# Optimization experiments

Measured on AMD Instinct MI355X. Metric: run time of the kernel, lower is better.

The kernel has to match this reference:

```python
import jax, jax.numpy as jnp
import numpy as np

SEQ = 4096
D_MODEL = 2048


def setup_inputs() -> dict:
    key = jax.random.key(0)
    k1, k2, k3, k4 = jax.random.split(key, 4)
    scale = 1.0 / np.sqrt(D_MODEL)
    token_encodings = jax.random.normal(k1, (SEQ, D_MODEL), dtype=jnp.float32)
    W_q = jax.random.normal(k2, (D_MODEL, D_MODEL), dtype=jnp.float32) * scale
    W_k = jax.random.normal(k3, (D_MODEL, D_MODEL), dtype=jnp.float32) * scale
    W_v = jax.random.normal(k4, (D_MODEL, D_MODEL), dtype=jnp.float32) * scale
    # causal mask: True where attention is disallowed (strictly upper triangular),
    # mirroring `mask = mask == 0` applied to a lower-triangular ones matrix.
    mask = jnp.triu(jnp.ones((SEQ, SEQ), dtype=bool), k=1)
    return {"token_encodings": token_encodings, "W_q": W_q, "W_k": W_k,
            "W_v": W_v, "mask": mask}


def reference(token_encodings, W_q, W_k, W_v, mask):
    # nn.Linear(bias=False): y = x @ W.T
    q = token_encodings @ W_q.T  # [S, D]
    k = token_encodings @ W_k.T  # [S, D]
    v = token_encodings @ W_v.T  # [S, D]
    sims = q @ k.T               # [S, S]
    scaled = sims / jnp.asarray(np.sqrt(D_MODEL), dtype=sims.dtype)
    scaled = jnp.where(mask, jnp.asarray(-1e9, dtype=scaled.dtype), scaled)
    attn = jax.nn.softmax(scaled, axis=1)
    return attn @ v              # [S, D]
```

## Files before the change

### kernel.cpp

```cpp
#include <hip/hip_runtime.h>
#include <hip/hip_bf16.h>

typedef unsigned short u16;
typedef __attribute__((ext_vector_type(8))) short short8;
typedef __attribute__((ext_vector_type(4))) float f32x4;
typedef __attribute__((ext_vector_type(4))) unsigned short u16x4;

#define SEQL 4096
#define DMOD 2048

__device__ __forceinline__ u16 f2bf(float x) {
    unsigned int u = __float_as_uint(x);
    u += 0x7FFF + ((u >> 16) & 1);
    return (u16)(u >> 16);
}

__device__ __forceinline__ float bf2f(u16 x) {
    return __uint_as_float(((unsigned)x) << 16);
}

__device__ __forceinline__ void async_copy16(const void* g, void* s) {
    __builtin_amdgcn_global_load_lds(
        (const __attribute__((address_space(1))) unsigned int*)g,
        (__attribute__((address_space(3))) unsigned int*)s,
        16, 0, 0);
}

__global__ __launch_bounds__(256)
void cast_f32_bf16(const float* __restrict__ in, u16* __restrict__ out, int n4) {
    int i = blockIdx.x * 256 + threadIdx.x;
    if (i >= n4) return;
    float4 v = ((const float4*)in)[i];
    u16x4 r;
    r[0] = f2bf(v.x); r[1] = f2bf(v.y); r[2] = f2bf(v.z); r[3] = f2bf(v.w);
    ((u16x4*)out)[i] = r;
}

__global__ __launch_bounds__(256)
void cast3_f32_bf16(const float* __restrict__ w0, const float* __restrict__ w1,
                    const float* __restrict__ w2, u16* __restrict__ o0,
                    u16* __restrict__ o1, u16* __restrict__ o2, int n4) {
    int i = blockIdx.x * 256 + threadIdx.x;
    if (i >= n4) return;
    const float* in = blockIdx.y == 0 ? w0 : blockIdx.y == 1 ? w1 : w2;
    u16* out        = blockIdx.y == 0 ? o0 : blockIdx.y == 1 ? o1 : o2;
    float4 v = ((const float4*)in)[i];
    u16x4 r;
    r[0] = f2bf(v.x); r[1] = f2bf(v.y); r[2] = f2bf(v.z); r[3] = f2bf(v.w);
    ((u16x4*)out)[i] = r;
}

__global__ __launch_bounds__(256)
void gemm_qkv64(const u16* __restrict__ A,
                const u16* __restrict__ B0, const u16* __restrict__ B1, const u16* __restrict__ B2,
                u16* __restrict__ C0, u16* __restrict__ C1, u16* __restrict__ C2)
{
    const int K = DMOD, N = DMOD;
    const int bid = blockIdx.x;
    const int e = bid & 7, idx = bid >> 3;
    const int br = idx / 6;
    const int bcAll = e * 6 + idx % 6;
    const int which = bcAll >> 4;
    const int rowBase = br * 128, colBase = (bcAll & 15) * 128;
    const u16* B = which == 0 ? B0 : which == 1 ? B1 : B2;
    u16*       C = which == 0 ? C0 : which == 1 ? C1 : C2;

    __shared__ __align__(16) u16 As[2][128 * 64];
    __shared__ __align__(16) u16 Bs[2][128 * 64];

    const int tid = threadIdx.x;
    const int wid = tid >> 6, lane = tid & 63;
    const int wr = wid >> 1, wc = wid & 1;
    const int q = lane >> 4, l15 = lane & 15;

    const int nkt = K >> 6;
    const u16* Ag = A + (size_t)rowBase * K;
    const u16* Bg = B + (size_t)colBase * K;
    const int srow = lane >> 3;
    const int scel = ((lane & 7) * 8) ^ (srow << 3);

    f32x4 acc[4][4] = {};

    auto stage = [&](int buf, int kt) {
        const int k0 = kt * 64;
        #pragma unroll
        for (int r = 0; r < 4; ++r) {
            const int rowl = wid * 32 + r * 8;
            async_copy16(Ag + (size_t)(rowl + srow) * K + k0 + scel, &As[buf][rowl * 64]);
            async_copy16(Bg + (size_t)(rowl + srow) * K + k0 + scel, &Bs[buf][rowl * 64]);
        }
    };

    stage(0, 0);
    for (int kt = 0; kt < nkt; ++kt) {
        const int cur = kt & 1;
        asm volatile("s_waitcnt vmcnt(0)" ::: "memory");
        __syncthreads();
        if (kt + 1 < nkt) stage(cur ^ 1, kt + 1);

        short8 af[2][4], bfr[2][4];
        #pragma unroll
        for (int ks = 0; ks < 2; ++ks) {
            #pragma unroll
            for (int m = 0; m < 4; ++m) {
                const int row = wr * 64 + m * 16 + l15;
                af[ks][m] = *(const short8*)&As[cur][row * 64 + ((ks * 32 + q * 8) ^ ((row & 7) << 3))];
            }
            #pragma unroll
            for (int n = 0; n < 4; ++n) {
                const int row = wc * 64 + n * 16 + l15;
                bfr[ks][n] = *(const short8*)&Bs[cur][row * 64 + ((ks * 32 + q * 8) ^ ((row & 7) << 3))];
            }
        }
        #pragma unroll
        for (int ks = 0; ks < 2; ++ks)
            #pragma unroll
            for (int m = 0; m < 4; ++m)
                #pragma unroll
                for (int n = 0; n < 4; ++n)
                    acc[m][n] = __builtin_amdgcn_mfma_f32_16x16x32_bf16(
                        af[ks][m], bfr[ks][n], acc[m][n], 0, 0, 0);
        __syncthreads();
    }

    const int crow0 = rowBase + wr * 64 + (lane >> 4) * 4;
    const int ccol0 = colBase + wc * 64 + l15;
    #pragma unroll
    for (int m = 0; m < 4; ++m)
        #pragma unroll
        for (int n = 0; n < 4; ++n)
            #pragma unroll
            for (int r = 0; r < 4; ++r)
                C[(size_t)(crow0 + m * 16 + r) * N + (ccol0 + n * 16)] = f2bf(acc[m][n][r]);
}

template<int MODE>
__global__ __launch_bounds__(256)
void gemm_bt64(const u16* __restrict__ A, const u16* __restrict__ B,
               void* __restrict__ Cout, const float* __restrict__ linv,
               int N, int K, float scale)
{
    int br, bc;
    if (MODE == 2) {
        const int bid = blockIdx.x;
        const int e = bid & 7, idx = bid >> 3;
        const int g = idx >> 1;
        br = (g < 16) ? (2 * g) : (63 - 2 * g);
        bc = e * 2 + (idx & 1);
    } else {
        br = blockIdx.y; bc = blockIdx.x;
        if (bc > br) return;
    }
    const int rowBase = br * 128, colBase = bc * 128;

    __shared__ __align__(16) u16 As[2][128 * 64];
    __shared__ __align__(16) u16 Bs[2][128 * 64];

    const int tid = threadIdx.x;
    const int wid = tid >> 6, lane = tid & 63;
    const int wr = wid >> 1, wc = wid & 1;
    const int q = lane >> 4, l15 = lane & 15;

    int nkt = K >> 6;
    if (MODE == 2) { const int lim = br * 2 + 2; if (lim < nkt) nkt = lim; }

    const u16* Ag = A + (size_t)rowBase * K;
    const u16* Bg = B + (size_t)colBase * K;
    const int srow = lane >> 3;
    const int scel = ((lane & 7) * 8) ^ (srow << 3);

    f32x4 acc[4][4] = {};

    auto stage = [&](int buf, int kt) {
        const int k0 = kt * 64;
        #pragma unroll
        for (int r = 0; r < 4; ++r) {
            const int rowl = wid * 32 + r * 8;
            async_copy16(Ag + (size_t)(rowl + srow) * K + k0 + scel, &As[buf][rowl * 64]);
            async_copy16(Bg + (size_t)(rowl + srow) * K + k0 + scel, &Bs[buf][rowl * 64]);
        }
    };

    stage(0, 0);
    for (int kt = 0; kt < nkt; ++kt) {
        const int cur = kt & 1;
        asm volatile("s_waitcnt vmcnt(0)" ::: "memory");
        __syncthreads();
        if (kt + 1 < nkt) stage(cur ^ 1, kt + 1);

        short8 af[2][4], bfr[2][4];
        #pragma unroll
        for (int ks = 0; ks < 2; ++ks) {
            #pragma unroll
            for (int m = 0; m < 4; ++m) {
                const int row = wr * 64 + m * 16 + l15;
                af[ks][m] = *(const short8*)&As[cur][row * 64 + ((ks * 32 + q * 8) ^ ((row & 7) << 3))];
            }
            #pragma unroll
            for (int n = 0; n < 4; ++n) {
                const int row = wc * 64 + n * 16 + l15;
                bfr[ks][n] = *(const short8*)&Bs[cur][row * 64 + ((ks * 32 + q * 8) ^ ((row & 7) << 3))];
            }
        }
        #pragma unroll
        for (int ks = 0; ks < 2; ++ks)
            #pragma unroll
            for (int m = 0; m < 4; ++m)
                #pragma unroll
                for (int n = 0; n < 4; ++n)
                    acc[m][n] = __builtin_amdgcn_mfma_f32_16x16x32_bf16(
                        af[ks][m], bfr[ks][n], acc[m][n], 0, 0, 0);
        __syncthreads();
    }

    const int crow0 = rowBase + wr * 64 + (lane >> 4) * 4;
    const int ccol0 = colBase + wc * 64 + l15;
    if (MODE == 1) {
        u16* E = (u16*)Cout;
        #pragma unroll
        for (int m = 0; m < 4; ++m)
            #pragma unroll
            for (int r = 0; r < 4; ++r) {
                const int row = crow0 + m * 16 + r;
                #pragma unroll
                for (int n = 0; n < 4; ++n) {
                    const int col = ccol0 + n * 16;
                    float e = (col > row) ? 0.f : __expf(acc[m][n][r] * scale);
                    E[(size_t)row * N + col] = f2bf(e);
                }
            }
    } else {
        float* C = (float*)Cout;
        #pragma unroll
        for (int m = 0; m < 4; ++m)
            #pragma unroll
            for (int r = 0; r < 4; ++r) {
                const int row = crow0 + m * 16 + r;
                const float inv = linv[row];
                #pragma unroll
                for (int n = 0; n < 4; ++n)
                    C[(size_t)row * N + (ccol0 + n * 16)] = acc[m][n][r] * inv;
            }
    }
}

__global__ __launch_bounds__(256)
void transpose_bf16(const u16* __restrict__ in, u16* __restrict__ out, int R, int C) {
    __shared__ u16 t[64][65];
    const int cb = blockIdx.x * 64, rb = blockIdx.y * 64;
    const int tx = threadIdx.x & 63, ty = threadIdx.x >> 6;
    #pragma unroll
    for (int i = 0; i < 16; ++i) {
        const int r = i * 4 + ty;
        t[r][tx] = in[(size_t)(rb + r) * C + cb + tx];
    }
    __syncthreads();
    #pragma unroll
    for (int i = 0; i < 16; ++i) {
        const int r = i * 4 + ty;
        out[(size_t)(cb + r) * R + rb + tx] = t[tx][r];
    }
}

__global__ __launch_bounds__(256)
void rowsum_inv(const u16* __restrict__ E, float* __restrict__ linv) {
    const int row = blockIdx.x, tid = threadIdx.x, lane = tid & 63, wid = tid >> 6;
    const int len = row + 1;
    const u16* e = E + (size_t)row * SEQL;
    float s = 0.f;
    const int n8 = len >> 3;
    for (int j = tid; j < n8; j += 256) {
        short8 v = ((const short8*)e)[j];
        #pragma unroll
        for (int k = 0; k < 8; ++k) s += bf2f((u16)v[k]);
    }
    for (int j = (n8 << 3) + tid; j < len; j += 256) s += bf2f(e[j]);
    #pragma unroll
    for (int o = 32; o; o >>= 1) s += __shfl_xor(s, o);
    __shared__ float red[4];
    if (lane == 0) red[wid] = s;
    __syncthreads();
    if (tid == 0) linv[row] = 1.f / (red[0] + red[1] + red[2] + red[3]);
}

extern "C" void kernel_launch(void* const* d_in, const int* in_sizes, int n_in,
                              void* d_out, int out_size, void* d_ws, size_t ws_size,
                              hipStream_t stream)
{
    const float* X  = (const float*)d_in[0];
    const float* Wq = (const float*)d_in[1];
    const float* Wk = (const float*)d_in[2];
    const float* Wv = (const float*)d_in[3];
    float* Out = (float*)d_out;

    char* ws = (char*)d_ws;
    const size_t MB = 1ull << 20;
    u16*   Xb   = (u16*)(ws + 0);
    u16*   Wqb  = (u16*)(ws + 16 * MB);
    u16*   Wkb  = (u16*)(ws + 24 * MB);
    u16*   Wvb  = (u16*)(ws + 32 * MB);
    u16*   E    = (u16*)(ws + 16 * MB);
    u16*   Qb   = (u16*)(ws + 48 * MB);
    u16*   Kb   = (u16*)(ws + 64 * MB);
    u16*   Vb   = (u16*)(ws + 80 * MB);
    float* linv = (float*)(ws + 96 * MB);

    const float scale = 0.022097086912079608f;

    cast_f32_bf16<<<SEQL * DMOD / 4 / 256, 256, 0, stream>>>(X, Xb, SEQL * DMOD / 4);
    cast3_f32_bf16<<<dim3(DMOD * DMOD / 4 / 256, 3), 256, 0, stream>>>(
        Wq, Wk, Wv, Wqb, Wkb, Wvb, DMOD * DMOD / 4);

    gemm_qkv64<<<1536, 256, 0, stream>>>(Xb, Wqb, Wkb, Wvb, Qb, Kb, Vb);

    dim3 gS(SEQL / 128, SEQL / 128);
    gemm_bt64<1><<<gS, 256, 0, stream>>>(Qb, Kb, E, nullptr, SEQL, DMOD, scale);

    u16* Vt = Xb;
    transpose_bf16<<<dim3(DMOD / 64, SEQL / 64), 256, 0, stream>>>(Vb, Vt, SEQL, DMOD);

    rowsum_inv<<<SEQL, 256, 0, stream>>>(E, linv);

    gemm_bt64<2><<<512, 256, 0, stream>>>(E, Vt, Out, linv, DMOD, SEQL, 0.f);
}
```

Measured before the change: 292.9 us.

## Fuse softmax row-sum into QK epilogue via atomics and merge cast kernels

The separate rowsum kernel, which re-read the bf16 exponent matrix, is removed. Row sums are now accumulated in the QK^T epilogue with a 16-lane shuffle reduction and one float atomicAdd per row segment, and the PV epilogue takes the reciprocal itself. The two cast kernels are merged into one launch, and a memset clears the sum buffer. This saves one kernel and a large read, at the cost of atomic contention and summing unrounded fp32 exps rather than the bf16 values actually used.

```diff
diff --git a/kernel.cpp b/kernel.cpp
--- a/kernel.cpp
+++ b/kernel.cpp
@@ -13,10 +13,6 @@
     unsigned int u = __float_as_uint(x);
     u += 0x7FFF + ((u >> 16) & 1);
     return (u16)(u >> 16);
-}
-
-__device__ __forceinline__ float bf2f(u16 x) {
-    return __uint_as_float(((unsigned)x) << 16);
 }
 
 __device__ __forceinline__ void async_copy16(const void* g, void* s) {
@@ -27,23 +23,21 @@
 }
 
 __global__ __launch_bounds__(256)
-void cast_f32_bf16(const float* __restrict__ in, u16* __restrict__ out, int n4) {
-    int i = blockIdx.x * 256 + threadIdx.x;
-    if (i >= n4) return;
-    float4 v = ((const float4*)in)[i];
-    u16x4 r;
-    r[0] = f2bf(v.x); r[1] = f2bf(v.y); r[2] = f2bf(v.z); r[3] = f2bf(v.w);
-    ((u16x4*)out)[i] = r;
-}
-
-__global__ __launch_bounds__(256)
-void cast3_f32_bf16(const float* __restrict__ w0, const float* __restrict__ w1,
-                    const float* __restrict__ w2, u16* __restrict__ o0,
-                    u16* __restrict__ o1, u16* __restrict__ o2, int n4) {
-    int i = blockIdx.x * 256 + threadIdx.x;
-    if (i >= n4) return;
-    const float* in = blockIdx.y == 0 ? w0 : blockIdx.y == 1 ? w1 : w2;
-    u16* out        = blockIdx.y == 0 ? o0 : blockIdx.y == 1 ? o1 : o2;
+void cast_all(const float* __restrict__ X,  const float* __restrict__ Wq,
+              const float* __restrict__ Wk, const float* __restrict__ Wv,
+              u16* __restrict__ Xb,  u16* __restrict__ Wqb,
+              u16* __restrict__ Wkb, u16* __restrict__ Wvb)
+{
+    const int b = blockIdx.x;
+    const float* in; u16* out; int i;
+    if (b < 8192) { in = X; out = Xb; i = b * 256 + threadIdx.x; }
+    else {
+        const int w  = (b - 8192) >> 12;
+        const int lb = (b - 8192) & 4095;
+        i = lb * 256 + threadIdx.x;
+        in  = w == 0 ? Wq  : w == 1 ? Wk  : Wv;
+        out = w == 0 ? Wqb : w == 1 ? Wkb : Wvb;
+    }
     float4 v = ((const float4*)in)[i];
     u16x4 r;
     r[0] = f2bf(v.x); r[1] = f2bf(v.y); r[2] = f2bf(v.z); r[3] = f2bf(v.w);
@@ -137,7 +131,7 @@
 template<int MODE>
 __global__ __launch_bounds__(256)
 void gemm_bt64(const u16* __restrict__ A, const u16* __restrict__ B,
-               void* __restrict__ Cout, const float* __restrict__ linv,
+               void* __restrict__ Cout, float* __restrict__ lsum,
                int N, int K, float scale)
 {
     int br, bc;
@@ -222,12 +216,19 @@
             #pragma unroll
             for (int r = 0; r < 4; ++r) {
                 const int row = crow0 + m * 16 + r;
+                float rs = 0.f;
                 #pragma unroll
                 for (int n = 0; n < 4; ++n) {
                     const int col = ccol0 + n * 16;
                     float e = (col > row) ? 0.f : __expf(acc[m][n][r] * scale);
                     E[(size_t)row * N + col] = f2bf(e);
+                    rs += e;
                 }
+                rs += __shfl_xor(rs, 1);
+                rs += __shfl_xor(rs, 2);
+                rs += __shfl_xor(rs, 4);
+                rs += __shfl_xor(rs, 8);
+                if (l15 == 0) atomicAdd(&lsum[row], rs);
             }
     } else {
         float* C = (float*)Cout;
@@ -236,7 +237,7 @@
             #pragma unroll
             for (int r = 0; r < 4; ++r) {
                 const int row = crow0 + m * 16 + r;
-                const float inv = linv[row];
+                const float inv = 1.0f / lsum[row];
                 #pragma unroll
                 for (int n = 0; n < 4; ++n)
                     C[(size_t)row * N + (ccol0 + n * 16)] = acc[m][n][r] * inv;
@@ -260,27 +261,6 @@
         const int r = i * 4 + ty;
         out[(size_t)(cb + r) * R + rb + tx] = t[tx][r];
     }
-}
-
-__global__ __launch_bounds__(256)
-void rowsum_inv(const u16* __restrict__ E, float* __restrict__ linv) {
-    const int row = blockIdx.x, tid = threadIdx.x, lane = tid & 63, wid = tid >> 6;
-    const int len = row + 1;
-    const u16* e = E + (size_t)row * SEQL;
-    float s = 0.f;
-    const int n8 = len >> 3;
-    for (int j = tid; j < n8; j += 256) {
-        short8 v = ((const short8*)e)[j];
-        #pragma unroll
-        for (int k = 0; k < 8; ++k) s += bf2f((u16)v[k]);
-    }
-    for (int j = (n8 << 3) + tid; j < len; j += 256) s += bf2f(e[j]);
-    #pragma unroll
-    for (int o = 32; o; o >>= 1) s += __shfl_xor(s, o);
-    __shared__ float red[4];
-    if (lane == 0) red[wid] = s;
-    __syncthreads();
-    if (tid == 0) linv[row] = 1.f / (red[0] + red[1] + red[2] + red[3]);
 }
 
 extern "C" void kernel_launch(void* const* d_in, const int* in_sizes, int n_in,
@@ -303,23 +283,21 @@
     u16*   Qb   = (u16*)(ws + 48 * MB);
     u16*   Kb   = (u16*)(ws + 64 * MB);
     u16*   Vb   = (u16*)(ws + 80 * MB);
-    float* linv = (float*)(ws + 96 * MB);
+    float* lsum = (float*)(ws + 96 * MB);
 
     const float scale = 0.022097086912079608f;
 
-    cast_f32_bf16<<<SEQL * DMOD / 4 / 256, 256, 0, stream>>>(X, Xb, SEQL * DMOD / 4);
-    cast3_f32_bf16<<<dim3(DMOD * DMOD / 4 / 256, 3), 256, 0, stream>>>(
-        Wq, Wk, Wv, Wqb, Wkb, Wvb, DMOD * DMOD / 4);
+    hipMemsetAsync(lsum, 0, SEQL * sizeof(float), stream);
+
+    cast_all<<<8192 + 3 * 4096, 256, 0, stream>>>(X, Wq, Wk, Wv, Xb, Wqb, Wkb, Wvb);
 
     gemm_qkv64<<<1536, 256, 0, stream>>>(Xb, Wqb, Wkb, Wvb, Qb, Kb, Vb);
 
     dim3 gS(SEQL / 128, SEQL / 128);
-    gemm_bt64<1><<<gS, 256, 0, stream>>>(Qb, Kb, E, nullptr, SEQL, DMOD, scale);
+    gemm_bt64<1><<<gS, 256, 0, stream>>>(Qb, Kb, E, lsum, SEQL, DMOD, scale);
 
     u16* Vt = Xb;
     transpose_bf16<<<dim3(DMOD / 64, SEQL / 64), 256, 0, stream>>>(Vb, Vt, SEQL, DMOD);
 
-    rowsum_inv<<<SEQL, 256, 0, stream>>>(E, linv);
-
-    gemm_bt64<2><<<512, 256, 0, stream>>>(E, Vt, Out, linv, DMOD, SEQL, 0.f);
-}
+    gemm_bt64<2><<<512, 256, 0, stream>>>(E, Vt, Out, lsum, DMOD, SEQL, 0.f);
+}
```

Result: no change. 295.1 us (+0.8%).
